# Performance work log

Measured on AMD Instinct MI355X. Metric: run time of the kernel, lower is better.

Reference implementation:

```python
import jax, jax.numpy as jnp
import numpy as np

B, T, DIM, H = 4, 2048, 512, 8
DECAY = 0.9

def setup_inputs():
    key = jax.random.key(0)
    ks = jax.random.split(key, 8)
    s = 1.0 / np.sqrt(DIM)
    def lin(k):
        return jax.random.normal(k, (DIM, DIM), jnp.float32) * s
    return {
        "q": jax.random.normal(ks[0], (B, T, DIM), jnp.float32),
        "k": jax.random.normal(ks[1], (B, T, DIM), jnp.float32),
        "v": jax.random.normal(ks[2], (B, T, DIM), jnp.float32),
        "Wa": lin(ks[3]), "ba": jnp.zeros((DIM,), jnp.float32),
        "Wb": lin(ks[4]), "bb": jnp.zeros((DIM,), jnp.float32),
        "Wg": lin(ks[5]), "bg": jnp.zeros((DIM,), jnp.float32),
        "Wo": lin(ks[6]), "bo": jnp.zeros((DIM,), jnp.float32),
    }

def _linear_scan(a, b):
    # h_t = a_t * h_{t-1} + b_t along time axis=1, via associative scan
    def combine(c1, c2):
        a1, b1 = c1
        a2, b2 = c2
        return a1 * a2, a2 * b1 + b2
    return jax.lax.associative_scan(combine, (a, b), axis=1)[1]

def reference(q, k, v, Wa, ba, Wb, bb, Wg, bg, Wo, bo):
    # --- Mamba-style selective scan on q (no residual) ---
    a = jax.nn.sigmoid(q @ Wa + ba)   # input-dependent decay [B,T,D]
    b = q @ Wb + bb                   # input injection       [B,T,D]
    h = _linear_scan(a, b)            # recurrent state       [B,T,D]
    g = jax.nn.sigmoid(q @ Wg + bg)   # gate
    m_out = (h * g) @ Wo + bo         # [B,T,D]

    # --- RetNet-style decay-weighted linear retention ---
    Dh = DIM // H
    qh = q.reshape(B, T, H, Dh)
    kh = k.reshape(B, T, H, Dh)
    vh = v.reshape(B, T, H, Dh)
    t = jnp.arange(T)
    delta = t[:, None] - t[None, :]           # t - s
    mask = delta >= 0                         # causal
    decay_mat = jnp.where(
        mask,
        jnp.exp(jnp.where(mask, delta, 0).astype(jnp.float32) * np.float32(np.log(DECAY))),
        0.0,
    )                                          # [T,T]
    scores = jnp.einsum('bthd,bshd->bhts', qh, kh) * decay_mat  # [B,H,T,T]
    r_out = jnp.einsum('bhts,bshd->bthd', scores, vh).reshape(B, T, DIM)

    return m_out + r_out
```

## Files before the change

### kernel.cpp

```cpp
#include <hip/hip_runtime.h>
#include <hip/hip_bf16.h>

typedef unsigned short u16;

#define BB 4
#define TT 2048
#define DIM 512
#define NH 8
#define DH 64
#define DECAY 0.9f

#define CC 64
#define NC 32
#define BHN 32

#define CHS 32
#define NSC 64

#define TM 128
#define TN 128
#define BK 64

#define SS 72

typedef __attribute__((ext_vector_type(8))) short bf16x8;
typedef __attribute__((ext_vector_type(4))) float f32x4;

__device__ __forceinline__ u16 f2bfu(float f) {
  union { float f; unsigned int u; } c; c.f = f;
  unsigned int u = c.u + 0x7FFFu + ((c.u >> 16) & 1u);
  return (u16)(u >> 16);
}
__device__ __forceinline__ float bf2f(u16 u) {
  union { unsigned int u; float f; } c; c.u = ((unsigned int)u) << 16;
  return c.f;
}

__device__ __forceinline__ void gl_lds16(const void* g, void* l) {
  __builtin_amdgcn_global_load_lds(
      (const __attribute__((address_space(1))) void*)g,
      (__attribute__((address_space(3))) void*)(unsigned int)(unsigned long long)l,
      16, 0, 0);
}

__device__ __forceinline__ void gemm_tile(
    int nTile, int mTile, const u16* __restrict__ A, const u16* __restrict__ Bt,
    const float* __restrict__ b0, const float* __restrict__ b1,
    const float* __restrict__ b2,
    u16* __restrict__ C0, u16* __restrict__ C1, u16* __restrict__ C2,
    int act_mask, u16* As, u16* Bs, int tid) {
  int wave = tid >> 6, lane = tid & 63;
  int group = (nTile * TN) >> 9;
  const float* bias = (group == 0) ? b0 : (group == 1) ? b1 : b2;
  u16* C = (group == 0) ? C0 : (group == 1) ? C1 : C2;
  int act = (act_mask >> group) & 1;

  int wm = (wave >> 1) * 64, wn = (wave & 1) * 64;
  int rowA = lane & 15, khalf = lane >> 4;

  f32x4 acc[4][4];
#pragma unroll
  for (int i = 0; i < 4; ++i)
#pragma unroll
    for (int j = 0; j < 4; ++j) acc[i][j] = (f32x4){0.f, 0.f, 0.f, 0.f};

  const u16* Abase = A + (size_t)mTile * TM * 512;
  const u16* Bbase = Bt + (size_t)nTile * TN * 512;

  for (int kk = 0; kk < 512; kk += BK) {
#pragma unroll
    for (int i = 0; i < 4; ++i) {
      int o = (wave * 4 + i) * 64 + lane;
      int row = o >> 3, gk = (o & 7) ^ (row & 7);
      gl_lds16(Abase + (size_t)row * 512 + kk + gk * 8, &As[o * 8]);
    }
#pragma unroll
    for (int i = 0; i < 4; ++i) {
      int o = (wave * 4 + i) * 64 + lane;
      int row = o >> 3, gk = (o & 7) ^ (row & 7);
      gl_lds16(Bbase + (size_t)row * 512 + kk + gk * 8, &Bs[o * 8]);
    }
    __syncthreads();
#pragma unroll
    for (int k0 = 0; k0 < 2; ++k0) {
      bf16x8 af[4], bfr[4];
#pragma unroll
      for (int mi = 0; mi < 4; ++mi) {
        int rr = wm + mi * 16 + rowA;
        int gk = k0 * 4 + khalf;
        int o = rr * 8 + (gk ^ (rr & 7));
        af[mi] = *(const bf16x8*)&As[o * 8];
      }
#pragma unroll
      for (int ni = 0; ni < 4; ++ni) {
        int rr = wn + ni * 16 + rowA;
        int gk = k0 * 4 + khalf;
        int o = rr * 8 + (gk ^ (rr & 7));
        bfr[ni] = *(const bf16x8*)&Bs[o * 8];
      }
#pragma unroll
      for (int mi = 0; mi < 4; ++mi)
#pragma unroll
        for (int ni = 0; ni < 4; ++ni)
          acc[mi][ni] = __builtin_amdgcn_mfma_f32_16x16x32_bf16(
              af[mi], bfr[ni], acc[mi][ni], 0, 0, 0);
    }
    __syncthreads();
  }
  int cloc = lane & 15, rq = (lane >> 4) * 4;
#pragma unroll
  for (int mi = 0; mi < 4; ++mi) {
#pragma unroll
    for (int r = 0; r < 4; ++r) {
      int m = mTile * TM + wm + mi * 16 + rq + r;
#pragma unroll
      for (int ni = 0; ni < 4; ++ni) {
        int n = (nTile * TN + wn + ni * 16 + cloc) & 511;
        float vv = acc[mi][ni][r] + bias[n];
        if (act) vv = 1.0f / (1.0f + __expf(-vv));
        C[(size_t)m * 512 + n] = f2bfu(vv);
      }
    }
  }
}

__device__ __forceinline__ void gemm_tile64(
    int nTile, int mTile, const u16* __restrict__ A, const u16* __restrict__ Bt,
    const float* __restrict__ bias, float* __restrict__ C,
    const u16* __restrict__ Radd, u16* As, u16* Bs, int tid) {
  int wave = tid >> 6, lane = tid & 63;
  int wm = wave * 32;
  int rowA = lane & 15, khalf = lane >> 4;

  f32x4 acc[2][4];
#pragma unroll
  for (int i = 0; i < 2; ++i)
#pragma unroll
    for (int j = 0; j < 4; ++j) acc[i][j] = (f32x4){0.f, 0.f, 0.f, 0.f};

  const u16* Abase = A + (size_t)mTile * TM * 512;
  const u16* Bbase = Bt + (size_t)nTile * 64 * 512;

  for (int kk = 0; kk < 512; kk += BK) {
#pragma unroll
    for (int i = 0; i < 4; ++i) {
      int o = (wave * 4 + i) * 64 + lane;
      int row = o >> 3, gk = (o & 7) ^ (row & 7);
      gl_lds16(Abase + (size_t)row * 512 + kk + gk * 8, &As[o * 8]);
    }
#pragma unroll
    for (int i = 0; i < 2; ++i) {
      int o = (wave * 2 + i) * 64 + lane;
      int row = o >> 3, gk = (o & 7) ^ (row & 7);
      gl_lds16(Bbase + (size_t)row * 512 + kk + gk * 8, &Bs[o * 8]);
    }
    __syncthreads();
#pragma unroll
    for (int k0 = 0; k0 < 2; ++k0) {
      bf16x8 af[2], bfr[4];
#pragma unroll
      for (int mi = 0; mi < 2; ++mi) {
        int rr = wm + mi * 16 + rowA;
        int gk = k0 * 4 + khalf;
        int o = rr * 8 + (gk ^ (rr & 7));
        af[mi] = *(const bf16x8*)&As[o * 8];
      }
#pragma unroll
      for (int ni = 0; ni < 4; ++ni) {
        int rr = ni * 16 + rowA;
        int gk = k0 * 4 + khalf;
        int o = rr * 8 + (gk ^ (rr & 7));
        bfr[ni] = *(const bf16x8*)&Bs[o * 8];
      }
#pragma unroll
      for (int mi = 0; mi < 2; ++mi)
#pragma unroll
        for (int ni = 0; ni < 4; ++ni)
          acc[mi][ni] = __builtin_amdgcn_mfma_f32_16x16x32_bf16(
              af[mi], bfr[ni], acc[mi][ni], 0, 0, 0);
    }
    __syncthreads();
  }
  int cloc = lane & 15, rq = (lane >> 4) * 4;
#pragma unroll
  for (int mi = 0; mi < 2; ++mi) {
#pragma unroll
    for (int r = 0; r < 4; ++r) {
      int m = mTile * TM + wm + mi * 16 + rq + r;
#pragma unroll
      for (int ni = 0; ni < 4; ++ni) {
        int n = nTile * 64 + ni * 16 + cloc;
        float vv = acc[mi][ni][r] + bias[n] + bf2f(Radd[(size_t)m * 512 + n]);
        C[(size_t)m * 512 + n] = vv;
      }
    }
  }
}

__global__ __launch_bounds__(256) void k1_prep_retkv(
    const float* __restrict__ q, u16* __restrict__ qbf,
    const float* __restrict__ W0, const float* __restrict__ W1,
    const float* __restrict__ W2, const float* __restrict__ W3,
    u16* __restrict__ Wt,
    const float* __restrict__ k, const float* __restrict__ v,
    u16* __restrict__ KVTb, u16* __restrict__ VTg, u16* __restrict__ kcb) {
  __shared__ __align__(16) u16 smem[2 * 64 * SS];
  __shared__ float t[32][33];
  int bx = blockIdx.x, tid = threadIdx.x;
  if (bx < 1024) {
    int bh = bx & 31, c = bx >> 5;
    int b = bh >> 3, h = bh & 7;
    int wave = tid >> 6, lane = tid & 63;
    u16* VT = smem;
    u16* KT = smem + 64 * SS;
    size_t base = ((size_t)(b * TT + c * CC)) * DIM + h * DH;
    int row = tid >> 2, part = tid & 3, e0 = part * 16;
    float w = __powf(DECAY, (float)(63 - row));
    __align__(16) u16 krow[16];
    {
      const float4* vs = (const float4*)(v + base + (size_t)row * DIM + e0);
      const float4* ks = (const float4*)(k + base + (size_t)row * DIM + e0);
#pragma unroll
      for (int u4 = 0; u4 < 4; ++u4) {
        float4 fv = vs[u4], fk = ks[u4];
        VT[(e0 + u4 * 4 + 0) * SS + row] = f2bfu(fv.x);
        VT[(e0 + u4 * 4 + 1) * SS + row] = f2bfu(fv.y);
        VT[(e0 + u4 * 4 + 2) * SS + row] = f2bfu(fv.z);
        VT[(e0 + u4 * 4 + 3) * SS + row] = f2bfu(fv.w);
        u16 k0s = f2bfu(fk.x * w), k1s = f2bfu(fk.y * w);
        u16 k2s = f2bfu(fk.z * w), k3s = f2bfu(fk.w * w);
        KT[(e0 + u4 * 4 + 0) * SS + row] = k0s;
        KT[(e0 + u4 * 4 + 1) * SS + row] = k1s;
        KT[(e0 + u4 * 4 + 2) * SS + row] = k2s;
        KT[(e0 + u4 * 4 + 3) * SS + row] = k3s;
        krow[u4 * 4 + 0] = k0s; krow[u4 * 4 + 1] = k1s;
        krow[u4 * 4 + 2] = k2s; krow[u4 * 4 + 3] = k3s;
      }
    }
    {
      u16* kdst = kcb + (((size_t)bh * NC + c) * 64 + row) * 64 + e0;
      *(uint4*)kdst = *(const uint4*)&krow[0];
      *(uint4*)(kdst + 8) = *(const uint4*)&krow[8];
    }
    __syncthreads();
    {
      int e = row;
      u16* dst = VTg + ((size_t)bh * 64 + e) * TT + c * 64 + part * 16;
      *(uint4*)dst = *(const uint4*)&VT[e * SS + part * 16];
      *(uint4*)(dst + 8) = *(const uint4*)&VT[e * SS + part * 16 + 8];
    }
    int wm = (wave >> 1) * 32, wn = (wave & 1) * 32;
    int rowA = lane & 15, khalf = lane >> 4;
    f32x4 acc[2][2];
#pragma unroll
    for (int i = 0; i < 2; ++i)
#pragma unroll
      for (int j = 0; j < 2; ++j) acc[i][j] = (f32x4){0.f, 0.f, 0.f, 0.f};
#pragma unroll
    for (int k0 = 0; k0 < 2; ++k0) {
      int gk = k0 * 4 + khalf;
      bf16x8 af[2], bfr[2];
#pragma unroll
      for (int mi = 0; mi < 2; ++mi)
        af[mi] = *(const bf16x8*)&VT[(wm + mi * 16 + rowA) * SS + gk * 8];
#pragma unroll
      for (int ni = 0; ni < 2; ++ni)
        bfr[ni] = *(const bf16x8*)&KT[(wn + ni * 16 + rowA) * SS + gk * 8];
#pragma unroll
      for (int mi = 0; mi < 2; ++mi)
#pragma unroll
        for (int ni = 0; ni < 2; ++ni)
          acc[mi][ni] = __builtin_amdgcn_mfma_f32_16x16x32_bf16(
              af[mi], bfr[ni], acc[mi][ni], 0, 0, 0);
    }
    int cloc = lane & 15, rq = (lane >> 4) * 4;
    u16* o = KVTb + ((size_t)(c * BHN + bh)) * 4096;
#pragma unroll
    for (int mi = 0; mi < 2; ++mi)
#pragma unroll
      for (int r = 0; r < 4; ++r) {
        int e = wm + mi * 16 + rq + r;
#pragma unroll
        for (int ni = 0; ni < 2; ++ni)
          o[e * 64 + (wn + ni * 16 + cloc)] = f2bfu(acc[mi][ni][r]);
      }
  } else if (bx < 2048) {
    int bx2 = bx - 1024;
    int m = bx2 >> 8, rem = bx2 & 255;
    int n0 = (rem & 15) * 32, k0 = (rem >> 4) * 32;
    const float* W = (m == 0) ? W0 : (m == 1) ? W1 : (m == 2) ? W2 : W3;
    int tx = tid & 31, ty = tid >> 5;
#pragma unroll
    for (int r = 0; r < 32; r += 8)
      t[ty + r][tx] = W[(size_t)(k0 + ty + r) * DIM + n0 + tx];
    __syncthreads();
    u16* o = Wt + (size_t)m * DIM * DIM;
#pragma unroll
    for (int r = 0; r < 32; r += 8)
      o[(size_t)(n0 + ty + r) * DIM + k0 + tx] = f2bfu(t[tx][ty + r]);
  } else {
    int i = (bx - 2048) * 256 + tid;
    float4 f = ((const float4*)q)[i];
    ushort4 u;
    u.x = f2bfu(f.x); u.y = f2bfu(f.y); u.z = f2bfu(f.z); u.w = f2bfu(f.w);
    ((ushort4*)qbf)[i] = u;
  }
}

__global__ __launch_bounds__(256) void k2_gemm1_retscan(
    const u16* __restrict__ qbf, const u16* __restrict__ WtAll,
    const float* __restrict__ ba, const float* __restrict__ bb,
    const float* __restrict__ bg,
    u16* __restrict__ Ab16, u16* __restrict__ Bb16, u16* __restrict__ Gb16,
    const u16* __restrict__ KVTb, u16* __restrict__ Ptb) {
  __shared__ __align__(16) u16 smem[TM * BK + TN * BK];
  int bx = blockIdx.x, tid = threadIdx.x;
  if (bx < 768) {
    int r = bx & 7, t6 = bx >> 3;
    int nT = t6 % 12, s = t6 / 12;
    int mT = (s << 3) | r;
    gemm_tile(nT, mT, qbf, WtAll, ba, bb, bg, Ab16, Bb16, Gb16,
              0b101, smem, smem + TM * BK, tid);
  } else {
    int gid = (bx - 768) * 256 + tid;
    int bh = gid >> 12, ed = gid & 4095;
    float carry = 0.f;
    const float dC = __powf(DECAY, (float)CC);
    for (int c = 0; c < NC; ++c) {
      size_t idx = ((size_t)(c * BHN + bh)) * 4096 + ed;
      Ptb[idx] = f2bfu(carry);
      carry = fmaf(dC, carry, bf2f(KVTb[idx]));
    }
  }
}

__global__ __launch_bounds__(256) void k3_retout_part(
    const u16* __restrict__ Ab16, const u16* __restrict__ Bb16,
    float* __restrict__ SA, float* __restrict__ SB,
    const u16* __restrict__ qbf, const u16* __restrict__ kcb,
    const u16* __restrict__ VTg, const u16* __restrict__ Ptb,
    u16* __restrict__ routb) {
  __shared__ __align__(16) u16 Sa[64 * SS];
  __shared__ float dp[66];
  __shared__ float dpi[64];
  int bx = blockIdx.x, tid = threadIdx.x;
  if (bx >= 1024) {
    int bxp = bx - 1024;
    int ci = bxp >> 3, grp = bxp & 7;
    int ch = grp * 256 + tid;
    int bb2 = ch >> 9, d = ch & 511;
    size_t base = ((size_t)bb2 * TT + ci * CHS) * DIM + d;
    float h = 0.f, pA = 1.f;
#pragma unroll
    for (int t = 0; t < CHS; ++t) {
      float av = bf2f(Ab16[base + (size_t)t * DIM]);
      float bv = bf2f(Bb16[base + (size_t)t * DIM]);
      h = fmaf(av, h, bv);
      pA *= av;
    }
    SA[ci * 2048 + ch] = pA;
    SB[ci * 2048 + ch] = h;
    return;
  }
  int bh = bx & 31, c = bx >> 5;
  int b = bh >> 3, h = bh & 7;
  int wave = tid >> 6, lane = tid & 63;
  size_t base = ((size_t)(b * TT + c * CC)) * DIM + h * DH;
  if (tid < 66) dp[tid] = __powf(DECAY, (float)tid);
  if (tid < 64) dpi[tid] = __powf(DECAY, (float)tid - 63.0f);

  int wm = (wave >> 1) * 32, wn = (wave & 1) * 32;
  int rowA = lane & 15, khalf = lane >> 4;

  bf16x8 afq[2][2];
#pragma unroll
  for (int k0 = 0; k0 < 2; ++k0)
#pragma unroll
    for (int mi = 0; mi < 2; ++mi)
      afq[k0][mi] = *(const bf16x8*)(qbf + base +
          (size_t)(wm + mi * 16 + rowA) * 512 + (k0 * 4 + khalf) * 8);
  const u16* kcbase = kcb + ((size_t)bh * NC + c) * 64 * 64;
  bf16x8 bfk[2][2];
#pragma unroll
  for (int k0 = 0; k0 < 2; ++k0)
#pragma unroll
    for (int ni = 0; ni < 2; ++ni)
      bfk[k0][ni] = *(const bf16x8*)(kcbase +
          (size_t)(wn + ni * 16 + rowA) * 64 + (k0 * 4 + khalf) * 8);

  f32x4 accS[2][2];
#pragma unroll
  for (int i = 0; i < 2; ++i)
#pragma unroll
    for (int j = 0; j < 2; ++j) accS[i][j] = (f32x4){0.f, 0.f, 0.f, 0.f};
#pragma unroll
  for (int k0 = 0; k0 < 2; ++k0)
#pragma unroll
    for (int mi = 0; mi < 2; ++mi)
#pragma unroll
      for (int ni = 0; ni < 2; ++ni)
        accS[mi][ni] = __builtin_amdgcn_mfma_f32_16x16x32_bf16(
            afq[k0][mi], bfk[k0][ni], accS[mi][ni], 0, 0, 0);
  __syncthreads();

  int cloc = lane & 15, rq = (lane >> 4) * 4;
#pragma unroll
  for (int mi = 0; mi < 2; ++mi)
#pragma unroll
    for (int ni = 0; ni < 2; ++ni)
#pragma unroll
      for (int r = 0; r < 4; ++r) {
        int i = wm + mi * 16 + rq + r;
        int j = wn + ni * 16 + cloc;
        float sv = (j <= i) ? accS[mi][ni][r] * dpi[i] : 0.f;
        Sa[i * SS + j] = f2bfu(sv);
      }
#pragma unroll
  for (int mi = 0; mi < 2; ++mi) {
    float s = dp[wm + mi * 16 + rowA + 1];
#pragma unroll
    for (int k0 = 0; k0 < 2; ++k0) {
      bf16x8 t = afq[k0][mi];
#pragma unroll
      for (int u = 0; u < 8; ++u)
        t[u] = (short)f2bfu(bf2f((u16)t[u]) * s);
      afq[k0][mi] = t;
    }
  }
  __syncthreads();

  f32x4 accO[2][2];
#pragma unroll
  for (int i = 0; i < 2; ++i)
#pragma unroll
    for (int j = 0; j < 2; ++j) accO[i][j] = (f32x4){0.f, 0.f, 0.f, 0.f};
#pragma unroll
  for (int k0 = 0; k0 < 4; ++k0) {
    bf16x8 af[2], bfv[2];
#pragma unroll
    for (int mi = 0; mi < 2; ++mi) {
      if (k0 < 2)
        af[mi] = *(const bf16x8*)&Sa[(wm + mi * 16 + rowA) * SS +
                                     (k0 * 4 + khalf) * 8];
      else
        af[mi] = afq[k0 - 2][mi];
    }
#pragma unroll
    for (int ni = 0; ni < 2; ++ni) {
      int e = wn + ni * 16 + rowA;
      if (k0 < 2)
        bfv[ni] = *(const bf16x8*)(VTg + ((size_t)bh * 64 + e) * TT + c * 64 +
                                   (k0 * 4 + khalf) * 8);
      else
        bfv[ni] = *(const bf16x8*)(Ptb + ((size_t)(c * BHN + bh)) * 4096 +
                                   e * 64 + ((k0 - 2) * 4 + khalf) * 8);
    }
#pragma unroll
    for (int mi = 0; mi < 2; ++mi)
#pragma unroll
      for (int ni = 0; ni < 2; ++ni)
        accO[mi][ni] = __builtin_amdgcn_mfma_f32_16x16x32_bf16(
            af[mi], bfv[ni], accO[mi][ni], 0, 0, 0);
  }
#pragma unroll
  for (int mi = 0; mi < 2; ++mi)
#pragma unroll
    for (int r = 0; r < 4; ++r) {
      int i = wm + mi * 16 + rq + r;
#pragma unroll
      for (int ni = 0; ni < 2; ++ni) {
        int e = wn + ni * 16 + cloc;
        routb[base + (size_t)i * 512 + e] = f2bfu(accO[mi][ni][r]);
      }
    }
}

__global__ __launch_bounds__(256) void k4_apply(
    const u16* __restrict__ Ab16, const u16* __restrict__ Bb16,
    const u16* __restrict__ g, const float* __restrict__ SA,
    const float* __restrict__ SB, u16* __restrict__ hg) {
  int bx = blockIdx.x, tid = threadIdx.x;
  int ci = bx >> 3, grp = bx & 7;
  int ch = grp * 256 + tid;
  int bb = ch >> 9, d = ch & 511;
  float carry = 0.f;
  for (int p = 0; p < ci; ++p)
    carry = fmaf(SA[p * 2048 + ch], carry, SB[p * 2048 + ch]);
  size_t base = ((size_t)bb * TT + ci * CHS) * DIM + d;
  float h = carry;
#pragma unroll
  for (int t = 0; t < CHS; ++t) {
    size_t idx = base + (size_t)t * DIM;
    h = fmaf(bf2f(Ab16[idx]), h, bf2f(Bb16[idx]));
    hg[idx] = f2bfu(h * bf2f(g[idx]));
  }
}

__global__ __launch_bounds__(256) void k5_gemm2(
    const u16* __restrict__ hgbf, const u16* __restrict__ Wto,
    const float* __restrict__ bo, float* __restrict__ out,
    const u16* __restrict__ routb) {
  __shared__ __align__(16) u16 smem[TM * BK + 64 * BK];
  int bx = blockIdx.x;
  int r = bx & 7, t6 = bx >> 3;
  int nT = t6 & 7, s = t6 >> 3;
  int mT = (s << 3) | r;
  gemm_tile64(nT, mT, hgbf, Wto, bo, out, routb,
              smem, smem + TM * BK, threadIdx.x);
}

extern "C" void kernel_launch(void* const* d_in, const int* in_sizes, int n_in,
                              void* d_out, int out_size, void* d_ws, size_t ws_size,
                              hipStream_t stream) {
  const float* q  = (const float*)d_in[0];
  const float* k  = (const float*)d_in[1];
  const float* v  = (const float*)d_in[2];
  const float* Wa = (const float*)d_in[3];
  const float* ba = (const float*)d_in[4];
  const float* Wb = (const float*)d_in[5];
  const float* bb = (const float*)d_in[6];
  const float* Wg = (const float*)d_in[7];
  const float* bg = (const float*)d_in[8];
  const float* Wo = (const float*)d_in[9];
  const float* bo = (const float*)d_in[10];
  float* out = (float*)d_out;
  float* ws = (float*)d_ws;

  const size_t NEL = (size_t)BB * TT * DIM;
  float* SA = ws;
  float* SB = SA + NSC * 2048;
  u16* up = (u16*)(SB + NSC * 2048);
  u16* Ab16  = up;  up += NEL;
  u16* Bb16  = up;  up += NEL;
  u16* Gb16  = up;  up += NEL;
  u16* qbf   = up;  up += NEL;
  u16* hgbf  = up;  up += NEL;
  u16* WtAll = up;  up += 4 * DIM * DIM;
  u16* KVTb  = up;  up += (size_t)NC * BHN * 4096;
  u16* Ptb   = up;  up += (size_t)NC * BHN * 4096;
  u16* VTg   = up;  up += (size_t)BHN * 64 * TT;
  u16* routb = up;  up += NEL;
  u16* kcb   = up;  up += (size_t)BHN * NC * 64 * 64;

  k1_prep_retkv<<<6144, 256, 0, stream>>>(q, qbf, Wa, Wb, Wg, Wo, WtAll,
                                          k, v, KVTb, VTg, kcb);

  k2_gemm1_retscan<<<1280, 256, 0, stream>>>(qbf, WtAll, ba, bb, bg,
                                             Ab16, Bb16, Gb16, KVTb, Ptb);

  k3_retout_part<<<1536, 256, 0, stream>>>(Ab16, Bb16, SA, SB,
                                           qbf, kcb, VTg, Ptb, routb);

  k4_apply<<<512, 256, 0, stream>>>(Ab16, Bb16, Gb16, SA, SB, hgbf);

  k5_gemm2<<<512, 256, 0, stream>>>(hgbf, WtAll + 3 * DIM * DIM,
                                    bo, out, routb);
}
```

Before: 174.4 us.

## Split retention output across scan-partial and scan-apply kernels to balance load

Moves the retention output blocks so half run alongside the chunk-partial scan in k3 and the other half alongside the scan-apply in k4, instead of all in k3 and none in k4. Device helpers are factored out for each work unit. The q-to-bf16 conversion now handles two float4 per thread, which reduces the k1 grid. The retention scan loop is unrolled. The aim is better overlap of the memory-bound scan work with the MFMA retention work in each launch, at the cost of more complex grid indexing.

```diff
diff --git a/kernel.cpp b/kernel.cpp
--- a/kernel.cpp
+++ b/kernel.cpp
@@ -195,6 +195,177 @@
       }
     }
   }
+}
+
+__device__ __forceinline__ void dev_retscan(int unit, int tid,
+    const u16* __restrict__ KVTb, u16* __restrict__ Ptb) {
+  int gid = unit * 256 + tid;
+  int bh = gid >> 12, ed = gid & 4095;
+  float carry = 0.f;
+  const float dC = __powf(DECAY, (float)CC);
+#pragma unroll
+  for (int c = 0; c < NC; ++c) {
+    size_t idx = ((size_t)(c * BHN + bh)) * 4096 + ed;
+    Ptb[idx] = f2bfu(carry);
+    carry = fmaf(dC, carry, bf2f(KVTb[idx]));
+  }
+}
+
+__device__ __forceinline__ void dev_part(int unit, int tid,
+    const u16* __restrict__ Ab16, const u16* __restrict__ Bb16,
+    float* __restrict__ SA, float* __restrict__ SB) {
+  int ci = unit >> 3, grp = unit & 7;
+  int ch = grp * 256 + tid;
+  int bb2 = ch >> 9, d = ch & 511;
+  size_t base = ((size_t)bb2 * TT + ci * CHS) * DIM + d;
+  float h = 0.f, pA = 1.f;
+#pragma unroll
+  for (int t = 0; t < CHS; ++t) {
+    float av = bf2f(Ab16[base + (size_t)t * DIM]);
+    float bv = bf2f(Bb16[base + (size_t)t * DIM]);
+    h = fmaf(av, h, bv);
+    pA *= av;
+  }
+  SA[ci * 2048 + ch] = pA;
+  SB[ci * 2048 + ch] = h;
+}
+
+__device__ __forceinline__ void dev_apply(int unit, int tid,
+    const u16* __restrict__ Ab16, const u16* __restrict__ Bb16,
+    const u16* __restrict__ g, const float* __restrict__ SA,
+    const float* __restrict__ SB, u16* __restrict__ hg) {
+  int ci = unit >> 3, grp = unit & 7;
+  int ch = grp * 256 + tid;
+  int bb = ch >> 9, d = ch & 511;
+  float carry = 0.f;
+  for (int p = 0; p < ci; ++p)
+    carry = fmaf(SA[p * 2048 + ch], carry, SB[p * 2048 + ch]);
+  size_t base = ((size_t)bb * TT + ci * CHS) * DIM + d;
+  float h = carry;
+#pragma unroll
+  for (int t = 0; t < CHS; ++t) {
+    size_t idx = base + (size_t)t * DIM;
+    h = fmaf(bf2f(Ab16[idx]), h, bf2f(Bb16[idx]));
+    hg[idx] = f2bfu(h * bf2f(g[idx]));
+  }
+}
+
+__device__ __forceinline__ void dev_retout(int unit, int tid,
+    u16* Sa, float* dp, float* dpi,
+    const u16* __restrict__ qbf, const u16* __restrict__ kcb,
+    const u16* __restrict__ VTg, const u16* __restrict__ Ptb,
+    u16* __restrict__ routb) {
+  int bh = unit & 31, c = unit >> 5;
+  int b = bh >> 3, h = bh & 7;
+  int wave = tid >> 6, lane = tid & 63;
+  size_t base = ((size_t)(b * TT + c * CC)) * DIM + h * DH;
+  if (tid < 66) dp[tid] = __powf(DECAY, (float)tid);
+  if (tid < 64) dpi[tid] = __powf(DECAY, (float)tid - 63.0f);
+
+  int wm = (wave >> 1) * 32, wn = (wave & 1) * 32;
+  int rowA = lane & 15, khalf = lane >> 4;
+
+  bf16x8 afq[2][2];
+#pragma unroll
+  for (int k0 = 0; k0 < 2; ++k0)
+#pragma unroll
+    for (int mi = 0; mi < 2; ++mi)
+      afq[k0][mi] = *(const bf16x8*)(qbf + base +
+          (size_t)(wm + mi * 16 + rowA) * 512 + (k0 * 4 + khalf) * 8);
+  const u16* kcbase = kcb + ((size_t)bh * NC + c) * 64 * 64;
+  bf16x8 bfk[2][2];
+#pragma unroll
+  for (int k0 = 0; k0 < 2; ++k0)
+#pragma unroll
+    for (int ni = 0; ni < 2; ++ni)
+      bfk[k0][ni] = *(const bf16x8*)(kcbase +
+          (size_t)(wn + ni * 16 + rowA) * 64 + (k0 * 4 + khalf) * 8);
+
+  f32x4 accS[2][2];
+#pragma unroll
+  for (int i = 0; i < 2; ++i)
+#pragma unroll
+    for (int j = 0; j < 2; ++j) accS[i][j] = (f32x4){0.f, 0.f, 0.f, 0.f};
+#pragma unroll
+  for (int k0 = 0; k0 < 2; ++k0)
+#pragma unroll
+    for (int mi = 0; mi < 2; ++mi)
+#pragma unroll
+      for (int ni = 0; ni < 2; ++ni)
+        accS[mi][ni] = __builtin_amdgcn_mfma_f32_16x16x32_bf16(
+            afq[k0][mi], bfk[k0][ni], accS[mi][ni], 0, 0, 0);
+  __syncthreads();
+
+  int cloc = lane & 15, rq = (lane >> 4) * 4;
+#pragma unroll
+  for (int mi = 0; mi < 2; ++mi)
+#pragma unroll
+    for (int ni = 0; ni < 2; ++ni)
+#pragma unroll
+      for (int r = 0; r < 4; ++r) {
+        int i = wm + mi * 16 + rq + r;
+        int j = wn + ni * 16 + cloc;
+        float sv = (j <= i) ? accS[mi][ni][r] * dpi[i] : 0.f;
+        Sa[i * SS + j] = f2bfu(sv);
+      }
+#pragma unroll
+  for (int mi = 0; mi < 2; ++mi) {
+    float s = dp[wm + mi * 16 + rowA + 1];
+#pragma unroll
+    for (int k0 = 0; k0 < 2; ++k0) {
+      bf16x8 t = afq[k0][mi];
+#pragma unroll
+      for (int u = 0; u < 8; ++u)
+        t[u] = (short)f2bfu(bf2f((u16)t[u]) * s);
+      afq[k0][mi] = t;
+    }
+  }
+  __syncthreads();
+
+  f32x4 accO[2][2];
+#pragma unroll
+  for (int i = 0; i < 2; ++i)
+#pragma unroll
+    for (int j = 0; j < 2; ++j) accO[i][j] = (f32x4){0.f, 0.f, 0.f, 0.f};
+#pragma unroll
+  for (int k0 = 0; k0 < 4; ++k0) {
+    bf16x8 af[2], bfv[2];
+#pragma unroll
+    for (int mi = 0; mi < 2; ++mi) {
+      if (k0 < 2)
+        af[mi] = *(const bf16x8*)&Sa[(wm + mi * 16 + rowA) * SS +
+                                     (k0 * 4 + khalf) * 8];
+      else
+        af[mi] = afq[k0 - 2][mi];
+    }
+#pragma unroll
+    for (int ni = 0; ni < 2; ++ni) {
+      int e = wn + ni * 16 + rowA;
+      if (k0 < 2)
+        bfv[ni] = *(const bf16x8*)(VTg + ((size_t)bh * 64 + e) * TT + c * 64 +
+                                   (k0 * 4 + khalf) * 8);
+      else
+        bfv[ni] = *(const bf16x8*)(Ptb + ((size_t)(c * BHN + bh)) * 4096 +
+                                   e * 64 + ((k0 - 2) * 4 + khalf) * 8);
+    }
+#pragma unroll
+    for (int mi = 0; mi < 2; ++mi)
+#pragma unroll
+      for (int ni = 0; ni < 2; ++ni)
+        accO[mi][ni] = __builtin_amdgcn_mfma_f32_16x16x32_bf16(
+            af[mi], bfv[ni], accO[mi][ni], 0, 0, 0);
+  }
+#pragma unroll
+  for (int mi = 0; mi < 2; ++mi)
+#pragma unroll
+    for (int r = 0; r < 4; ++r) {
+      int i = wm + mi * 16 + rq + r;
+#pragma unroll
+      for (int ni = 0; ni < 2; ++ni) {
+        int e = wn + ni * 16 + cloc;
+        routb[base + (size_t)i * 512 + e] = f2bfu(accO[mi][ni][r]);
+      }
+    }
 }
 
 __global__ __launch_bounds__(256) void k1_prep_retkv(
@@ -299,11 +470,14 @@
     for (int r = 0; r < 32; r += 8)
       o[(size_t)(n0 + ty + r) * DIM + k0 + tx] = f2bfu(t[tx][ty + r]);
   } else {
-    int i = (bx - 2048) * 256 + tid;
-    float4 f = ((const float4*)q)[i];
-    ushort4 u;
-    u.x = f2bfu(f.x); u.y = f2bfu(f.y); u.z = f2bfu(f.z); u.w = f2bfu(f.w);
-    ((ushort4*)qbf)[i] = u;
+    int i0 = ((bx - 2048) * 256 + tid) * 2;
+#pragma unroll
+    for (int u2 = 0; u2 < 2; ++u2) {
+      float4 f = ((const float4*)q)[i0 + u2];
+      ushort4 u;
+      u.x = f2bfu(f.x); u.y = f2bfu(f.y); u.z = f2bfu(f.z); u.w = f2bfu(f.w);
+      ((ushort4*)qbf)[i0 + u2] = u;
+    }
   }
 }
 
@@ -322,19 +496,11 @@
     gemm_tile(nT, mT, qbf, WtAll, ba, bb, bg, Ab16, Bb16, Gb16,
               0b101, smem, smem + TM * BK, tid);
   } else {
-    int gid = (bx - 768) * 256 + tid;
-    int bh = gid >> 12, ed = gid & 4095;
-    float carry = 0.f;
-    const float dC = __powf(DECAY, (float)CC);
-    for (int c = 0; c < NC; ++c) {
-      size_t idx = ((size_t)(c * BHN + bh)) * 4096 + ed;
-      Ptb[idx] = f2bfu(carry);
-      carry = fmaf(dC, carry, bf2f(KVTb[idx]));
-    }
-  }
-}
-
-__global__ __launch_bounds__(256) void k3_retout_part(
+    dev_retscan(bx - 768, tid, KVTb, Ptb);
+  }
+}
+
+__global__ __launch_bounds__(256) void k3_part_retout(
     const u16* __restrict__ Ab16, const u16* __restrict__ Bb16,
     float* __restrict__ SA, float* __restrict__ SB,
     const u16* __restrict__ qbf, const u16* __restrict__ kcb,
@@ -344,156 +510,29 @@
   __shared__ float dp[66];
   __shared__ float dpi[64];
   int bx = blockIdx.x, tid = threadIdx.x;
-  if (bx >= 1024) {
-    int bxp = bx - 1024;
-    int ci = bxp >> 3, grp = bxp & 7;
-    int ch = grp * 256 + tid;
-    int bb2 = ch >> 9, d = ch & 511;
-    size_t base = ((size_t)bb2 * TT + ci * CHS) * DIM + d;
-    float h = 0.f, pA = 1.f;
-#pragma unroll
-    for (int t = 0; t < CHS; ++t) {
-      float av = bf2f(Ab16[base + (size_t)t * DIM]);
-      float bv = bf2f(Bb16[base + (size_t)t * DIM]);
-      h = fmaf(av, h, bv);
-      pA *= av;
-    }
-    SA[ci * 2048 + ch] = pA;
-    SB[ci * 2048 + ch] = h;
+  if (bx < 512) {
+    dev_part(bx, tid, Ab16, Bb16, SA, SB);
     return;
   }
-  int bh = bx & 31, c = bx >> 5;
-  int b = bh >> 3, h = bh & 7;
-  int wave = tid >> 6, lane = tid & 63;
-  size_t base = ((size_t)(b * TT + c * CC)) * DIM + h * DH;
-  if (tid < 66) dp[tid] = __powf(DECAY, (float)tid);
-  if (tid < 64) dpi[tid] = __powf(DECAY, (float)tid - 63.0f);
-
-  int wm = (wave >> 1) * 32, wn = (wave & 1) * 32;
-  int rowA = lane & 15, khalf = lane >> 4;
-
-  bf16x8 afq[2][2];
-#pragma unroll
-  for (int k0 = 0; k0 < 2; ++k0)
-#pragma unroll
-    for (int mi = 0; mi < 2; ++mi)
-      afq[k0][mi] = *(const bf16x8*)(qbf + base +
-          (size_t)(wm + mi * 16 + rowA) * 512 + (k0 * 4 + khalf) * 8);
-  const u16* kcbase = kcb + ((size_t)bh * NC + c) * 64 * 64;
-  bf16x8 bfk[2][2];
-#pragma unroll
-  for (int k0 = 0; k0 < 2; ++k0)
-#pragma unroll
-    for (int ni = 0; ni < 2; ++ni)
-      bfk[k0][ni] = *(const bf16x8*)(kcbase +
-          (size_t)(wn + ni * 16 + rowA) * 64 + (k0 * 4 + khalf) * 8);
-
-  f32x4 accS[2][2];
-#pragma unroll
-  for (int i = 0; i < 2; ++i)
-#pragma unroll
-    for (int j = 0; j < 2; ++j) accS[i][j] = (f32x4){0.f, 0.f, 0.f, 0.f};
-#pragma unroll
-  for (int k0 = 0; k0 < 2; ++k0)
-#pragma unroll
-    for (int mi = 0; mi < 2; ++mi)
-#pragma unroll
-      for (int ni = 0; ni < 2; ++ni)
-        accS[mi][ni] = __builtin_amdgcn_mfma_f32_16x16x32_bf16(
-            afq[k0][mi], bfk[k0][ni], accS[mi][ni], 0, 0, 0);
-  __syncthreads();
-
-  int cloc = lane & 15, rq = (lane >> 4) * 4;
-#pragma unroll
-  for (int mi = 0; mi < 2; ++mi)
-#pragma unroll
-    for (int ni = 0; ni < 2; ++ni)
-#pragma unroll
-      for (int r = 0; r < 4; ++r) {
-        int i = wm + mi * 16 + rq + r;
-        int j = wn + ni * 16 + cloc;
-        float sv = (j <= i) ? accS[mi][ni][r] * dpi[i] : 0.f;
-        Sa[i * SS + j] = f2bfu(sv);
-      }
-#pragma unroll
-  for (int mi = 0; mi < 2; ++mi) {
-    float s = dp[wm + mi * 16 + rowA + 1];
-#pragma unroll
-    for (int k0 = 0; k0 < 2; ++k0) {
-      bf16x8 t = afq[k0][mi];
-#pragma unroll
-      for (int u = 0; u < 8; ++u)
-        t[u] = (short)f2bfu(bf2f((u16)t[u]) * s);
-      afq[k0][mi] = t;
-    }
-  }
-  __syncthreads();
-
-  f32x4 accO[2][2];
-#pragma unroll
-  for (int i = 0; i < 2; ++i)
-#pragma unroll
-    for (int j = 0; j < 2; ++j) accO[i][j] = (f32x4){0.f, 0.f, 0.f, 0.f};
-#pragma unroll
-  for (int k0 = 0; k0 < 4; ++k0) {
-    bf16x8 af[2], bfv[2];
-#pragma unroll
-    for (int mi = 0; mi < 2; ++mi) {
-      if (k0 < 2)
-        af[mi] = *(const bf16x8*)&Sa[(wm + mi * 16 + rowA) * SS +
-                                     (k0 * 4 + khalf) * 8];
-      else
-        af[mi] = afq[k0 - 2][mi];
-    }
-#pragma unroll
-    for (int ni = 0; ni < 2; ++ni) {
-      int e = wn + ni * 16 + rowA;
-      if (k0 < 2)
-        bfv[ni] = *(const bf16x8*)(VTg + ((size_t)bh * 64 + e) * TT + c * 64 +
-                                   (k0 * 4 + khalf) * 8);
-      else
-        bfv[ni] = *(const bf16x8*)(Ptb + ((size_t)(c * BHN + bh)) * 4096 +
-                                   e * 64 + ((k0 - 2) * 4 + khalf) * 8);
-    }
-#pragma unroll
-    for (int mi = 0; mi < 2; ++mi)
-#pragma unroll
-      for (int ni = 0; ni < 2; ++ni)
-        accO[mi][ni] = __builtin_amdgcn_mfma_f32_16x16x32_bf16(
-            af[mi], bfv[ni], accO[mi][ni], 0, 0, 0);
-  }
-#pragma unroll
-  for (int mi = 0; mi < 2; ++mi)
-#pragma unroll
-    for (int r = 0; r < 4; ++r) {
-      int i = wm + mi * 16 + rq + r;
-#pragma unroll
-      for (int ni = 0; ni < 2; ++ni) {
-        int e = wn + ni * 16 + cloc;
-        routb[base + (size_t)i * 512 + e] = f2bfu(accO[mi][ni][r]);
-      }
-    }
-}
-
-__global__ __launch_bounds__(256) void k4_apply(
+  dev_retout(bx - 512, tid, Sa, dp, dpi, qbf, kcb, VTg, Ptb, routb);
+}
+
+__global__ __launch_bounds__(256) void k4_apply_retout(
     const u16* __restrict__ Ab16, const u16* __restrict__ Bb16,
     const u16* __restrict__ g, const float* __restrict__ SA,
-    const float* __restrict__ SB, u16* __restrict__ hg) {
+    const float* __restrict__ SB, u16* __restrict__ hg,
+    const u16* __restrict__ qbf, const u16* __restrict__ kcb,
+    const u16* __restrict__ VTg, const u16* __restrict__ Ptb,
+    u16* __restrict__ routb) {
+  __shared__ __align__(16) u16 Sa[64 * SS];
+  __shared__ float dp[66];
+  __shared__ float dpi[64];
   int bx = blockIdx.x, tid = threadIdx.x;
-  int ci = bx >> 3, grp = bx & 7;
-  int ch = grp * 256 + tid;
-  int bb = ch >> 9, d = ch & 511;
-  float carry = 0.f;
-  for (int p = 0; p < ci; ++p)
-    carry = fmaf(SA[p * 2048 + ch], carry, SB[p * 2048 + ch]);
-  size_t base = ((size_t)bb * TT + ci * CHS) * DIM + d;
-  float h = carry;
-#pragma unroll
-  for (int t = 0; t < CHS; ++t) {
-    size_t idx = base + (size_t)t * DIM;
-    h = fmaf(bf2f(Ab16[idx]), h, bf2f(Bb16[idx]));
-    hg[idx] = f2bfu(h * bf2f(g[idx]));
-  }
+  if (bx < 512) {
+    dev_apply(bx, tid, Ab16, Bb16, g, SA, SB, hg);
+    return;
+  }
+  dev_retout(bx, tid, Sa, dp, dpi, qbf, kcb, VTg, Ptb, routb);
 }
 
 __global__ __launch_bounds__(256) void k5_gemm2(
@@ -528,8 +567,8 @@
 
   const size_t NEL = (size_t)BB * TT * DIM;
   float* SA = ws;
-  float* SB = SA + NSC * 2048;
-  u16* up = (u16*)(SB + NSC * 2048);
+  float* SB = SA + (size_t)NSC * 2048;
+  u16* up = (u16*)(SB + (size_t)NSC * 2048);
   u16* Ab16  = up;  up += NEL;
   u16* Bb16  = up;  up += NEL;
   u16* Gb16  = up;  up += NEL;
@@ -542,16 +581,17 @@
   u16* routb = up;  up += NEL;
   u16* kcb   = up;  up += (size_t)BHN * NC * 64 * 64;
 
-  k1_prep_retkv<<<6144, 256, 0, stream>>>(q, qbf, Wa, Wb, Wg, Wo, WtAll,
+  k1_prep_retkv<<<4096, 256, 0, stream>>>(q, qbf, Wa, Wb, Wg, Wo, WtAll,
                                           k, v, KVTb, VTg, kcb);
 
   k2_gemm1_retscan<<<1280, 256, 0, stream>>>(qbf, WtAll, ba, bb, bg,
                                              Ab16, Bb16, Gb16, KVTb, Ptb);
 
-  k3_retout_part<<<1536, 256, 0, stream>>>(Ab16, Bb16, SA, SB,
+  k3_part_retout<<<1024, 256, 0, stream>>>(Ab16, Bb16, SA, SB,
                                            qbf, kcb, VTg, Ptb, routb);
 
-  k4_apply<<<512, 256, 0, stream>>>(Ab16, Bb16, Gb16, SA, SB, hgbf);
+  k4_apply_retout<<<1024, 256, 0, stream>>>(Ab16, Bb16, Gb16, SA, SB, hgbf,
+                                            qbf, kcb, VTg, Ptb, routb);
 
   k5_gemm2<<<512, 256, 0, stream>>>(hgbf, WtAll + 3 * DIM * DIM,
                                     bo, out, routb);
```

Measured after the change: 176.5 us. No clear change (+1.1%).
